# Kernel tuning notes

Hardware: AMD Instinct MI355X
Metric: run time of the kernel (lower is better)

The kernel has to match this reference:

```python
import jax, jax.numpy as jnp
import numpy as np

N_NODES = 100000
N_EDGES = 1600000
D_IN = 128
D_OUT = 128


def setup_inputs() -> dict:
    key = jax.random.key(0)
    k1, k2, k3, k4 = jax.random.split(key, 4)
    x = jax.random.normal(k1, (N_NODES, D_IN), dtype=jnp.float32)
    # Xavier-uniform-like init for weight (exact distribution irrelevant for correctness baseline)
    weight = jax.random.normal(k2, (D_IN, D_OUT), dtype=jnp.float32) * (1.0 / np.sqrt(D_IN))
    bias = jnp.zeros((D_OUT,), dtype=jnp.float32)
    edge_index = jax.random.randint(k3, (2, N_EDGES), 0, N_NODES, dtype=jnp.int64 if jax.config.read('jax_enable_x64') else jnp.int32)
    edge_weight = jax.random.uniform(k4, (N_EDGES,), dtype=jnp.float32)
    return {"x": x, "weight": weight, "bias": bias,
            "edge_index": edge_index, "edge_weight": edge_weight}


def reference(x, weight, bias, edge_index, edge_weight):
    # support = X @ W   -- dense projection [N, D_out]
    support = x @ weight
    # output = A @ support -- SpMM via gather + weighted segment-sum
    src = edge_index[1]  # column index of adj (neighbor being aggregated)
    dst = edge_index[0]  # row index of adj (node receiving the message)
    messages = support[src] * edge_weight[:, None]          # [E, D_out]
    out = jax.ops.segment_sum(messages, dst, num_segments=N_NODES)  # [N, D_out]
    return out + bias
```

## Files before the change

kernel.cpp:

```cpp
#include <hip/hip_runtime.h>
#include <hip/hip_bf16.h>

#define N_NODES 100000
#define N_EDGES 1600000
#define D 128

#define NBUK 1024
#define BSH 7
#define CAP 2560
#define CAP_H 1344
#define NAGG2 (((N_NODES + 127) >> BSH) * 2)
#define NSCAT 256
#define PA_EPB 6250
#define EPT 7
#define SRC_MASK 0x01FFFFFF

#define QMAX 7.5f
#define QINV (127.0f / QMAX)
#define QSC  (QMAX / 127.0f)

typedef __attribute__((ext_vector_type(8))) short bf16x8;
typedef __attribute__((ext_vector_type(4))) float f32x4;

static __device__ __forceinline__ short f2bf(float f) {
    unsigned u = __builtin_bit_cast(unsigned, f);
    u += 0x7FFFu + ((u >> 16) & 1u);
    return (short)(u >> 16);
}

__global__ void wt_kernel(const float* __restrict__ w, short* __restrict__ wt,
                          int* __restrict__ gcur) {
    const int i = blockIdx.x * blockDim.x + threadIdx.x;
    if (i < D * D) {
        const int k = i / D, c = i % D;
        wt[c * D + k] = f2bf(w[i]);
    }
    if (i < NBUK) gcur[i] = 0;
}

__global__ __launch_bounds__(256) void gemm_quant_kernel(
    const float* __restrict__ x, const short* __restrict__ wt,
    unsigned char* __restrict__ sup8u) {
    const int wid = blockIdx.x * 4 + (threadIdx.x >> 6);
    if (wid >= N_NODES / 16) return;
    const int l = threadIdx.x & 63;
    const int r = l & 15, g = l >> 4;
    const size_t row0 = (size_t)wid * 16;

    bf16x8 a[4];
    const float* xp = x + (row0 + r) * D + g * 8;
#pragma unroll
    for (int ks = 0; ks < 4; ++ks) {
        const float4 f0 = *reinterpret_cast<const float4*>(xp + ks * 32);
        const float4 f1 = *reinterpret_cast<const float4*>(xp + ks * 32 + 4);
        bf16x8 t;
        t[0] = f2bf(f0.x); t[1] = f2bf(f0.y); t[2] = f2bf(f0.z); t[3] = f2bf(f0.w);
        t[4] = f2bf(f1.x); t[5] = f2bf(f1.y); t[6] = f2bf(f1.z); t[7] = f2bf(f1.w);
        a[ks] = t;
    }

    f32x4 acc[8];
#pragma unroll
    for (int nt = 0; nt < 8; ++nt) {
        acc[nt] = (f32x4){0.f, 0.f, 0.f, 0.f};
        const short* wp = wt + (size_t)(nt * 16 + r) * D + g * 8;
#pragma unroll
        for (int ks = 0; ks < 4; ++ks) {
            const bf16x8 b = *reinterpret_cast<const bf16x8*>(wp + ks * 32);
            acc[nt] = __builtin_amdgcn_mfma_f32_16x16x32_bf16(a[ks], b, acc[nt],
                                                              0, 0, 0);
        }
    }

#pragma unroll
    for (int q = 0; q < 4; ++q) {
        unsigned char* sp = sup8u + (row0 + g * 4 + q) * D + r;
#pragma unroll
        for (int nt = 0; nt < 8; ++nt) {
            float v = acc[nt][q] * QINV;
            v = fmaxf(-127.f, fminf(127.f, v));
            sp[nt * 16] = (unsigned char)(__float2int_rn(v) + 128);
        }
    }
}

__global__ __launch_bounds__(1024) void bukscatter_kernel(
    const int* __restrict__ dst, const int* __restrict__ src,
    const float* __restrict__ ew, int* __restrict__ gcur,
    int2* __restrict__ inter_sw) {
    __shared__ int h[NBUK];
    const int t = threadIdx.x;
    if (t < NBUK) h[t] = 0;
    __syncthreads();
    const int beg = blockIdx.x * PA_EPB;
    const int end = min(beg + PA_EPB, N_EDGES);

    int dv[EPT], sv[EPT];
    float wv[EPT];
    bool ok[EPT];

#pragma unroll
    for (int u = 0; u < EPT; ++u) {
        const int idx = beg + u * 1024 + t;
        ok[u] = (idx < end);
        if (ok[u]) {
            dv[u] = dst[idx];
            sv[u] = src[idx];
            wv[u] = ew[idx];
            atomicAdd(&h[dv[u] >> BSH], 1);
        }
    }
    __syncthreads();

    if (t < NBUK) {
        const int c = h[t];
        h[t] = c ? (t * CAP + atomicAdd(&gcur[t], c)) : 0;
    }
    __syncthreads();

#pragma unroll
    for (int u = 0; u < EPT; ++u) {
        if (ok[u]) {
            const int pos = atomicAdd(&h[dv[u] >> BSH], 1);
            inter_sw[pos] = make_int2(sv[u] | ((dv[u] & 127) << 25),
                                      __float_as_int(wv[u]));
        }
    }
}

__global__ __launch_bounds__(512) void sortagg_kernel(
    const int* __restrict__ gcur, const int2* __restrict__ inter_sw,
    const unsigned char* __restrict__ sup8u, const float* __restrict__ bias,
    float* __restrict__ out) {
    __shared__ int2 eb[CAP_H];
    __shared__ int st[64];
    __shared__ int cur[64];
    const int b = blockIdx.x, t = threadIdx.x;
    const int cb = b >> 1, hf = b & 1;
    const int cnt = gcur[cb];
    const int2* in = inter_sw + (size_t)cb * CAP;

    if (t < 64) st[t] = 0;
    __syncthreads();

    int2 e0, e1, e2, e3, e4;
    bool k0 = false, k1 = false, k2 = false, k3 = false, k4 = false;
    const int i0 = t, i1 = t + 512, i2 = t + 1024, i3 = t + 1536, i4 = t + 2048;
    if (i0 < cnt) { e0 = in[i0]; const int d7 = (unsigned)e0.x >> 25; if ((d7 >> 6) == hf) { k0 = true; atomicAdd(&st[d7 & 63], 1); } }
    if (i1 < cnt) { e1 = in[i1]; const int d7 = (unsigned)e1.x >> 25; if ((d7 >> 6) == hf) { k1 = true; atomicAdd(&st[d7 & 63], 1); } }
    if (i2 < cnt) { e2 = in[i2]; const int d7 = (unsigned)e2.x >> 25; if ((d7 >> 6) == hf) { k2 = true; atomicAdd(&st[d7 & 63], 1); } }
    if (i3 < cnt) { e3 = in[i3]; const int d7 = (unsigned)e3.x >> 25; if ((d7 >> 6) == hf) { k3 = true; atomicAdd(&st[d7 & 63], 1); } }
    if (i4 < cnt) { e4 = in[i4]; const int d7 = (unsigned)e4.x >> 25; if ((d7 >> 6) == hf) { k4 = true; atomicAdd(&st[d7 & 63], 1); } }
    __syncthreads();

    if (t < 64) {
        const int hv = st[t];
        int s = hv;
#pragma unroll
        for (int o = 1; o < 64; o <<= 1) {
            const int v = __shfl_up(s, o);
            if (t >= o) s += v;
        }
        st[t] = s - hv;
        cur[t] = s - hv;
    }
    __syncthreads();

    if (k0) eb[atomicAdd(&cur[((unsigned)e0.x >> 25) & 63], 1)] = make_int2(e0.x & SRC_MASK, e0.y);
    if (k1) eb[atomicAdd(&cur[((unsigned)e1.x >> 25) & 63], 1)] = make_int2(e1.x & SRC_MASK, e1.y);
    if (k2) eb[atomicAdd(&cur[((unsigned)e2.x >> 25) & 63], 1)] = make_int2(e2.x & SRC_MASK, e2.y);
    if (k3) eb[atomicAdd(&cur[((unsigned)e3.x >> 25) & 63], 1)] = make_int2(e3.x & SRC_MASK, e3.y);
    if (k4) eb[atomicAdd(&cur[((unsigned)e4.x >> 25) & 63], 1)] = make_int2(e4.x & SRC_MASK, e4.y);
    __syncthreads();

    const int wv = t >> 6, lane = t & 63;
    const int g = lane >> 4;
    const int fl = lane & 15;
    const int node0 = (cb << BSH) + (hf << 6);

    const float4 b0 = *reinterpret_cast<const float4*>(&bias[fl * 8]);
    const float4 b1 = *reinterpret_cast<const float4*>(&bias[fl * 8 + 4]);

    for (int k = 0; k < 8; ++k) {
        const int nl = wv * 8 + k;
        const int node = node0 + nl;
        if (node >= N_NODES) break;
        const int beg = st[nl], end = cur[nl];

        float acc[8] = {0, 0, 0, 0, 0, 0, 0, 0};
        float W = 0.f;
        for (int i = beg + g; i < end; i += 4) {
            const int2 sw = eb[i];
            const float w = __int_as_float(sw.y);
            const uint2 v = *reinterpret_cast<const uint2*>(
                &sup8u[(size_t)sw.x * D + fl * 8]);
            W += w;
#pragma unroll
            for (int q = 0; q < 4; ++q) {
                acc[q]     = fmaf(w, (float)((v.x >> (8 * q)) & 0xFFu), acc[q]);
                acc[4 + q] = fmaf(w, (float)((v.y >> (8 * q)) & 0xFFu), acc[4 + q]);
            }
        }
#pragma unroll
        for (int q = 0; q < 8; ++q) {
            acc[q] += __shfl_xor(acc[q], 16);
            acc[q] += __shfl_xor(acc[q], 32);
        }
        W += __shfl_xor(W, 16);
        W += __shfl_xor(W, 32);
        if (g == 0) {
            const float wb = 128.0f * W;
            float* o = &out[(size_t)node * D + fl * 8];
            reinterpret_cast<float4*>(o)[0] =
                make_float4(fmaf(acc[0] - wb, QSC, b0.x),
                            fmaf(acc[1] - wb, QSC, b0.y),
                            fmaf(acc[2] - wb, QSC, b0.z),
                            fmaf(acc[3] - wb, QSC, b0.w));
            reinterpret_cast<float4*>(o)[1] =
                make_float4(fmaf(acc[4] - wb, QSC, b1.x),
                            fmaf(acc[5] - wb, QSC, b1.y),
                            fmaf(acc[6] - wb, QSC, b1.z),
                            fmaf(acc[7] - wb, QSC, b1.w));
        }
    }
}

extern "C" void kernel_launch(void* const* d_in, const int* in_sizes, int n_in,
                              void* d_out, int out_size, void* d_ws, size_t ws_size,
                              hipStream_t stream) {
    const float* x      = (const float*)d_in[0];
    const float* weight = (const float*)d_in[1];
    const float* bias   = (const float*)d_in[2];
    const int*   eidx   = (const int*)d_in[3];
    const float* ew     = (const float*)d_in[4];
    float* out = (float*)d_out;

    const int* dst_idx = eidx;
    const int* src_idx = eidx + N_EDGES;

    char* p = (char*)d_ws;
    unsigned char* sup8u = (unsigned char*)p; p += (size_t)N_NODES * D;
    short* wt        = (short*)p;  p += (size_t)D * D * 2;
    int*   gcur      = (int*)p;    p += NBUK * 4;
    int2*  inter_sw  = (int2*)p;   p += (size_t)NBUK * CAP * 8;

    wt_kernel<<<(D * D + 255) / 256, 256, 0, stream>>>(weight, wt, gcur);

    gemm_quant_kernel<<<(N_NODES / 16 + 3) / 4, 256, 0, stream>>>(x, wt, sup8u);

    bukscatter_kernel<<<NSCAT, 1024, 0, stream>>>(dst_idx, src_idx, ew, gcur,
                                                  inter_sw);

    sortagg_kernel<<<NAGG2, 512, 0, stream>>>(gcur, inter_sw, sup8u, bias, out);
}
```

Baseline: 111.9 us.

## Split buckets into two half-node subbuckets filled from opposite ends

The bucket scatter now bins edges into 64-node sub-buckets. Even halves are filled forward from the start of each 128-node bucket region and odd halves backward from its end, with separate global counters. Each aggregation block then reads only the edges for its own half, not the whole bucket filtered by a half flag. This roughly halves the global reads and per-edge filtering work in sortagg, at the cost of a larger shared histogram and twice as many global atomics in the scatter.

```diff
diff --git a/kernel.cpp b/kernel.cpp
--- a/kernel.cpp
+++ b/kernel.cpp
@@ -6,6 +6,7 @@
 #define D 128
 
 #define NBUK 1024
+#define NSUB 2048
 #define BSH 7
 #define CAP 2560
 #define CAP_H 1344
@@ -29,13 +30,13 @@
 }
 
 __global__ void wt_kernel(const float* __restrict__ w, short* __restrict__ wt,
-                          int* __restrict__ gcur) {
+                          int* __restrict__ gcur01) {
     const int i = blockIdx.x * blockDim.x + threadIdx.x;
     if (i < D * D) {
         const int k = i / D, c = i % D;
         wt[c * D + k] = f2bf(w[i]);
     }
-    if (i < NBUK) gcur[i] = 0;
+    if (i < 2 * NBUK) gcur01[i] = 0;
 }
 
 __global__ __launch_bounds__(256) void gemm_quant_kernel(
@@ -86,11 +87,12 @@
 
 __global__ __launch_bounds__(1024) void bukscatter_kernel(
     const int* __restrict__ dst, const int* __restrict__ src,
-    const float* __restrict__ ew, int* __restrict__ gcur,
+    const float* __restrict__ ew, int* __restrict__ gcur01,
     int2* __restrict__ inter_sw) {
-    __shared__ int h[NBUK];
+    __shared__ int h[NSUB];
     const int t = threadIdx.x;
-    if (t < NBUK) h[t] = 0;
+    h[t] = 0;
+    h[t + 1024] = 0;
     __syncthreads();
     const int beg = blockIdx.x * PA_EPB;
     const int end = min(beg + PA_EPB, N_EDGES);
@@ -107,21 +109,34 @@
             dv[u] = dst[idx];
             sv[u] = src[idx];
             wv[u] = ew[idx];
-            atomicAdd(&h[dv[u] >> BSH], 1);
-        }
-    }
-    __syncthreads();
-
-    if (t < NBUK) {
-        const int c = h[t];
-        h[t] = c ? (t * CAP + atomicAdd(&gcur[t], c)) : 0;
+            atomicAdd(&h[dv[u] >> 6], 1);
+        }
+    }
+    __syncthreads();
+
+#pragma unroll
+    for (int j = 0; j < 2; ++j) {
+        const int sb = t + j * 1024;
+        const int c = h[sb];
+        if (c) {
+            const int cb = sb >> 1;
+            if ((sb & 1) == 0) {
+                const int base = atomicAdd(&gcur01[cb], c);
+                h[sb] = cb * CAP + base;
+            } else {
+                const int base = atomicAdd(&gcur01[NBUK + cb], c);
+                h[sb] = cb * CAP + CAP - 1 - base;
+            }
+        }
     }
     __syncthreads();
 
 #pragma unroll
     for (int u = 0; u < EPT; ++u) {
         if (ok[u]) {
-            const int pos = atomicAdd(&h[dv[u] >> BSH], 1);
+            const int sb = dv[u] >> 6;
+            const int pos = (sb & 1) ? atomicSub(&h[sb], 1)
+                                     : atomicAdd(&h[sb], 1);
             inter_sw[pos] = make_int2(sv[u] | ((dv[u] & 127) << 25),
                                       __float_as_int(wv[u]));
         }
@@ -129,7 +144,7 @@
 }
 
 __global__ __launch_bounds__(512) void sortagg_kernel(
-    const int* __restrict__ gcur, const int2* __restrict__ inter_sw,
+    const int* __restrict__ gcur01, const int2* __restrict__ inter_sw,
     const unsigned char* __restrict__ sup8u, const float* __restrict__ bias,
     float* __restrict__ out) {
     __shared__ int2 eb[CAP_H];
@@ -137,20 +152,17 @@
     __shared__ int cur[64];
     const int b = blockIdx.x, t = threadIdx.x;
     const int cb = b >> 1, hf = b & 1;
-    const int cnt = gcur[cb];
-    const int2* in = inter_sw + (size_t)cb * CAP;
+    const int cnt = hf ? gcur01[NBUK + cb] : gcur01[cb];
+    const int2* in = inter_sw + (size_t)cb * CAP + (hf ? (CAP - cnt) : 0);
 
     if (t < 64) st[t] = 0;
     __syncthreads();
 
-    int2 e0, e1, e2, e3, e4;
-    bool k0 = false, k1 = false, k2 = false, k3 = false, k4 = false;
-    const int i0 = t, i1 = t + 512, i2 = t + 1024, i3 = t + 1536, i4 = t + 2048;
-    if (i0 < cnt) { e0 = in[i0]; const int d7 = (unsigned)e0.x >> 25; if ((d7 >> 6) == hf) { k0 = true; atomicAdd(&st[d7 & 63], 1); } }
-    if (i1 < cnt) { e1 = in[i1]; const int d7 = (unsigned)e1.x >> 25; if ((d7 >> 6) == hf) { k1 = true; atomicAdd(&st[d7 & 63], 1); } }
-    if (i2 < cnt) { e2 = in[i2]; const int d7 = (unsigned)e2.x >> 25; if ((d7 >> 6) == hf) { k2 = true; atomicAdd(&st[d7 & 63], 1); } }
-    if (i3 < cnt) { e3 = in[i3]; const int d7 = (unsigned)e3.x >> 25; if ((d7 >> 6) == hf) { k3 = true; atomicAdd(&st[d7 & 63], 1); } }
-    if (i4 < cnt) { e4 = in[i4]; const int d7 = (unsigned)e4.x >> 25; if ((d7 >> 6) == hf) { k4 = true; atomicAdd(&st[d7 & 63], 1); } }
+    int2 e0, e1, e2;
+    const int i0 = t, i1 = t + 512, i2 = t + 1024;
+    if (i0 < cnt) { e0 = in[i0]; atomicAdd(&st[((unsigned)e0.x >> 25) & 63], 1); }
+    if (i1 < cnt) { e1 = in[i1]; atomicAdd(&st[((unsigned)e1.x >> 25) & 63], 1); }
+    if (i2 < cnt) { e2 = in[i2]; atomicAdd(&st[((unsigned)e2.x >> 25) & 63], 1); }
     __syncthreads();
 
     if (t < 64) {
@@ -166,11 +178,9 @@
     }
     __syncthreads();
 
-    if (k0) eb[atomicAdd(&cur[((unsigned)e0.x >> 25) & 63], 1)] = make_int2(e0.x & SRC_MASK, e0.y);
-    if (k1) eb[atomicAdd(&cur[((unsigned)e1.x >> 25) & 63], 1)] = make_int2(e1.x & SRC_MASK, e1.y);
-    if (k2) eb[atomicAdd(&cur[((unsigned)e2.x >> 25) & 63], 1)] = make_int2(e2.x & SRC_MASK, e2.y);
-    if (k3) eb[atomicAdd(&cur[((unsigned)e3.x >> 25) & 63], 1)] = make_int2(e3.x & SRC_MASK, e3.y);
-    if (k4) eb[atomicAdd(&cur[((unsigned)e4.x >> 25) & 63], 1)] = make_int2(e4.x & SRC_MASK, e4.y);
+    if (i0 < cnt) eb[atomicAdd(&cur[((unsigned)e0.x >> 25) & 63], 1)] = make_int2(e0.x & SRC_MASK, e0.y);
+    if (i1 < cnt) eb[atomicAdd(&cur[((unsigned)e1.x >> 25) & 63], 1)] = make_int2(e1.x & SRC_MASK, e1.y);
+    if (i2 < cnt) eb[atomicAdd(&cur[((unsigned)e2.x >> 25) & 63], 1)] = make_int2(e2.x & SRC_MASK, e2.y);
     __syncthreads();
 
     const int wv = t >> 6, lane = t & 63;
@@ -241,15 +251,15 @@
     char* p = (char*)d_ws;
     unsigned char* sup8u = (unsigned char*)p; p += (size_t)N_NODES * D;
     short* wt        = (short*)p;  p += (size_t)D * D * 2;
-    int*   gcur      = (int*)p;    p += NBUK * 4;
+    int*   gcur01    = (int*)p;    p += 2 * NBUK * 4;
     int2*  inter_sw  = (int2*)p;   p += (size_t)NBUK * CAP * 8;
 
-    wt_kernel<<<(D * D + 255) / 256, 256, 0, stream>>>(weight, wt, gcur);
+    wt_kernel<<<(D * D + 255) / 256, 256, 0, stream>>>(weight, wt, gcur01);
 
     gemm_quant_kernel<<<(N_NODES / 16 + 3) / 4, 256, 0, stream>>>(x, wt, sup8u);
 
-    bukscatter_kernel<<<NSCAT, 1024, 0, stream>>>(dst_idx, src_idx, ew, gcur,
+    bukscatter_kernel<<<NSCAT, 1024, 0, stream>>>(dst_idx, src_idx, ew, gcur01,
                                                   inter_sw);
 
-    sortagg_kernel<<<NAGG2, 512, 0, stream>>>(gcur, inter_sw, sup8u, bias, out);
-}
+    sortagg_kernel<<<NAGG2, 512, 0, stream>>>(gcur01, inter_sw, sup8u, bias, out);
+}
```

After: 115.0 us. 1.03x slower.
